# Kernel optimization log

Measured on AMD Instinct MI355X. Metric: run time of the kernel, lower is better.

The kernel has to match this reference:

```python
import jax, jax.numpy as jnp
import numpy as np

B, S, H = 64, 2048, 512


def setup_inputs() -> dict:
    key = jax.random.key(0)
    ks = jax.random.split(key, 7)
    sc = 1.0 / np.sqrt(H)
    return {
        "encoder_outputs": jax.random.normal(ks[0], (B, S, H), dtype=jnp.float32),
        "hidden": jax.random.normal(ks[1], (B, H), dtype=jnp.float32),
        "W1": jax.random.uniform(ks[2], (H, H), jnp.float32, -sc, sc),
        "b1": jax.random.uniform(ks[3], (H,), jnp.float32, -sc, sc),
        "W2": jax.random.uniform(ks[4], (H, H), jnp.float32, -sc, sc),
        "b2": jax.random.uniform(ks[5], (H,), jnp.float32, -sc, sc),
        "V": jax.random.uniform(ks[6], (H, 1), jnp.float32, -sc, sc),
        "bV": jnp.zeros((1,), dtype=jnp.float32),
    }


def reference(encoder_outputs, hidden, W1, b1, W2, b2, V, bV):
    # score: tanh(W1(enc) + W2(hidden)) ; hidden broadcast over seq dim (no repeat materialized)
    proj_enc = jnp.einsum("bsh,hk->bsk", encoder_outputs, W1) + b1          # [B,S,H]
    proj_hid = (hidden @ W2 + b2)[:, None, :]                                 # [B,1,H]
    score = jnp.tanh(proj_enc + proj_hid)                                     # [B,S,H]
    logits = jnp.einsum("bsh,hk->bsk", score, V) + bV                        # [B,S,1]
    attention_weights = jax.nn.softmax(logits, axis=1)                        # softmax over seq
    context = jnp.sum(attention_weights * encoder_outputs, axis=1)            # [B,H]
    return context, attention_weights
```

## Files before the change

### kernel.cpp

```cpp
#include <hip/hip_runtime.h>
#include <hip/hip_bf16.h>
#include <cstdint>
#include <cstddef>

#define B_ 64
#define S_ 2048
#define H_ 512

typedef __bf16 bf16x8 __attribute__((ext_vector_type(8)));
typedef float  f32x4  __attribute__((ext_vector_type(4)));

#define AS_GLB __attribute__((address_space(1)))
#define AS_LDS __attribute__((address_space(3)))

__device__ __forceinline__ float fast_tanh(float x) {
    float e = __expf(2.0f * x);
    return 1.0f - __fdividef(2.0f, e + 1.0f);
}

__global__ __launch_bounds__(256) void w1t_kernel(const float* __restrict__ W1,
                                                  unsigned short* __restrict__ Wt) {
    __shared__ float tile[32][33];
    int tn = blockIdx.x >> 4;
    int tk = blockIdx.x & 15;
    int lx = threadIdx.x & 31;
    int ly = threadIdx.x >> 5;
#pragma unroll
    for (int i = 0; i < 4; ++i) {
        int k = tk * 32 + ly + i * 8;
        tile[ly + i * 8][lx] = W1[k * H_ + tn * 32 + lx];
    }
    __syncthreads();
#pragma unroll
    for (int i = 0; i < 4; ++i) {
        int n = tn * 32 + ly + i * 8;
        float v = tile[lx][ly + i * 8];
        __bf16 bv = (__bf16)v;
        Wt[(size_t)n * H_ + tk * 32 + lx] = *(unsigned short*)&bv;
    }
}

__global__ __launch_bounds__(512) void hidproj_kernel(const float* __restrict__ hidden,
                                                      const float* __restrict__ W2,
                                                      const float* __restrict__ b1,
                                                      const float* __restrict__ b2,
                                                      float* __restrict__ cvals) {
    int b = blockIdx.x;
    int h = threadIdx.x;
    float acc = b1[h] + b2[h];
    const float* hp = hidden + b * H_;
    const float* wp = W2 + h;
#pragma unroll 8
    for (int k = 0; k < H_; ++k) acc = fmaf(hp[k], wp[(size_t)k * H_], acc);
    cvals[b * H_ + h] = acc;
}

__global__ __launch_bounds__(256) void score_kernel(const float* __restrict__ enc,
                                                    const unsigned short* __restrict__ Wt,
                                                    const float* __restrict__ cvals,
                                                    const float* __restrict__ Vp,
                                                    float* __restrict__ logits) {
    __shared__ unsigned short As[2][128][64];
    __shared__ unsigned short Bs[2][128][64];

    int orig = blockIdx.x;
    int wg   = (orig & 7) * 512 + (orig >> 3);
    int b     = wg >> 6;
    int stile = (wg >> 2) & 15;
    int ntile = wg & 3;

    int tid  = threadIdx.x;
    int wid  = tid >> 6;
    int lane = tid & 63;
    int wm = wid >> 1, wn = wid & 1;

    f32x4 acc[4][4];
#pragma unroll
    for (int m = 0; m < 4; ++m)
#pragma unroll
        for (int n = 0; n < 4; ++n) acc[m][n] = (f32x4){0.f, 0.f, 0.f, 0.f};

    const float* Abase = enc + ((size_t)(b * S_ + stile * 128)) * H_;
    float4 ra[4][2];

    auto stageA_load = [&](int kt) {
        int kk = kt * 64;
#pragma unroll
        for (int i = 0; i < 4; ++i) {
            int slot = tid + i * 256;
            int row  = slot >> 3;
            int c0   = (slot & 7) * 8;
            const float* p = Abase + (size_t)row * H_ + kk + c0;
            ra[i][0] = *(const float4*)p;
            ra[i][1] = *(const float4*)(p + 4);
        }
    };
    auto stageA_write = [&](int nb) {
#pragma unroll
        for (int i = 0; i < 4; ++i) {
            int slot = tid + i * 256;
            int row  = slot >> 3;
            int c0   = (slot & 7) * 8;
            bf16x8 v;
            const float* f = (const float*)&ra[i][0];
#pragma unroll
            for (int j = 0; j < 8; ++j) v[j] = (__bf16)f[j];
            *(bf16x8*)&As[nb][row][c0] = v;
        }
    };
    auto stageB = [&](int nb, int kt) {
        int kk = kt * 64;
#pragma unroll
        for (int i = 0; i < 4; ++i) {
            int chunk = wid * 4 + i;
            int n  = chunk * 8 + (lane >> 3);
            int c0 = (lane & 7) * 8;
            const unsigned short* src = Wt + (size_t)(ntile * 128 + n) * H_ + kk + c0;
            __builtin_amdgcn_global_load_lds((const AS_GLB unsigned int*)src,
                                             (AS_LDS unsigned int*)&Bs[nb][chunk * 8][0],
                                             16, 0, 0);
        }
    };
    auto compute = [&](int cb) {
#pragma unroll
        for (int ks = 0; ks < 2; ++ks) {
            int kof  = ks * 32 + (lane >> 4) * 8;
            int rsel = lane & 15;
            bf16x8 af[4], bfr[4];
#pragma unroll
            for (int m = 0; m < 4; ++m)
                af[m] = *(const bf16x8*)&As[cb][wm * 64 + m * 16 + rsel][kof];
#pragma unroll
            for (int n = 0; n < 4; ++n)
                bfr[n] = *(const bf16x8*)&Bs[cb][wn * 64 + n * 16 + rsel][kof];
#pragma unroll
            for (int m = 0; m < 4; ++m)
#pragma unroll
                for (int n = 0; n < 4; ++n)
                    acc[m][n] = __builtin_amdgcn_mfma_f32_16x16x32_bf16(
                        af[m], bfr[n], acc[m][n], 0, 0, 0);
        }
    };

    stageA_load(0);
    stageA_write(0);
    stageB(0, 0);
    __syncthreads();

    for (int kt = 0; kt < 8; ++kt) {
        int cur = kt & 1;
        if (kt < 7) {
            stageA_load(kt + 1);
            stageB(cur ^ 1, kt + 1);
        }
        compute(cur);
        if (kt < 7) stageA_write(cur ^ 1);
        __syncthreads();
    }

    int csel = lane & 15;
    float cw[4], vv[4];
#pragma unroll
    for (int n = 0; n < 4; ++n) {
        int col = ntile * 128 + wn * 64 + n * 16 + csel;
        cw[n] = cvals[b * H_ + col];
        vv[n] = Vp[col];
    }
    float part[16];
#pragma unroll
    for (int m = 0; m < 4; ++m)
#pragma unroll
        for (int r = 0; r < 4; ++r) {
            float p = 0.f;
#pragma unroll
            for (int n = 0; n < 4; ++n) {
                float s = fast_tanh(acc[m][n][r] + cw[n]);
                p = fmaf(vv[n], s, p);
            }
            part[m * 4 + r] = p;
        }
#pragma unroll
    for (int i = 0; i < 16; ++i)
#pragma unroll
        for (int off = 1; off < 16; off <<= 1)
            part[i] += __shfl_xor(part[i], off);

    if (csel == 0) {
        int g = lane >> 4;
#pragma unroll
        for (int m = 0; m < 4; ++m)
#pragma unroll
            for (int r = 0; r < 4; ++r) {
                int row = stile * 128 + wm * 64 + m * 16 + g * 4 + r;
                atomicAdd(&logits[b * S_ + row], part[m * 4 + r]);
            }
    }
}

__global__ __launch_bounds__(256) void softmax_kernel(const float* __restrict__ logits,
                                                      float* __restrict__ wout) {
    int b = blockIdx.x;
    int t = threadIdx.x;
    __shared__ float red[8];
    float v[8];
#pragma unroll
    for (int i = 0; i < 8; ++i) v[i] = logits[b * S_ + t + i * 256];
    float m = v[0];
#pragma unroll
    for (int i = 1; i < 8; ++i) m = fmaxf(m, v[i]);
#pragma unroll
    for (int off = 32; off >= 1; off >>= 1) m = fmaxf(m, __shfl_xor(m, off));
    int wid = t >> 6, lane = t & 63;
    if (lane == 0) red[wid] = m;
    __syncthreads();
    m = fmaxf(fmaxf(red[0], red[1]), fmaxf(red[2], red[3]));
    float s = 0.f;
#pragma unroll
    for (int i = 0; i < 8; ++i) { v[i] = __expf(v[i] - m); s += v[i]; }
#pragma unroll
    for (int off = 32; off >= 1; off >>= 1) s += __shfl_xor(s, off);
    if (lane == 0) red[4 + wid] = s;
    __syncthreads();
    float tot = red[4] + red[5] + red[6] + red[7];
    float inv = __fdividef(1.0f, tot);
#pragma unroll
    for (int i = 0; i < 8; ++i) wout[b * S_ + t + i * 256] = v[i] * inv;
}

__global__ __launch_bounds__(512) void context_kernel(const float* __restrict__ enc,
                                                      const float* __restrict__ w,
                                                      float* __restrict__ ctx) {
    int b  = blockIdx.x >> 4;
    int sc = blockIdx.x & 15;
    int h  = threadIdx.x;
    const float* ep = enc + ((size_t)(b * S_ + sc * 128)) * H_ + h;
    const float* wp = w + b * S_ + sc * 128;
    float acc = 0.f;
#pragma unroll 4
    for (int i = 0; i < 128; ++i) acc = fmaf(wp[i], ep[(size_t)i * H_], acc);
    atomicAdd(&ctx[b * H_ + h], acc);
}

extern "C" void kernel_launch(void* const* d_in, const int* in_sizes, int n_in,
                              void* d_out, int out_size, void* d_ws, size_t ws_size,
                              hipStream_t stream) {
    (void)in_sizes; (void)n_in; (void)out_size; (void)ws_size;
    const float* enc    = (const float*)d_in[0];
    const float* hidden = (const float*)d_in[1];
    const float* W1     = (const float*)d_in[2];
    const float* b1     = (const float*)d_in[3];
    const float* W2     = (const float*)d_in[4];
    const float* b2     = (const float*)d_in[5];
    const float* Vp     = (const float*)d_in[6];

    char* ws = (char*)d_ws;
    unsigned short* Wt = (unsigned short*)ws;
    float* cvals  = (float*)(ws + 524288);
    float* logits = (float*)(ws + 524288 + 131072);

    float* ctx  = (float*)d_out;
    float* wout = ctx + B_ * H_;

    hipMemsetAsync(logits, 0, (size_t)B_ * S_ * sizeof(float), stream);
    hipMemsetAsync(ctx,    0, (size_t)B_ * H_ * sizeof(float), stream);

    w1t_kernel<<<256, 256, 0, stream>>>(W1, Wt);
    hidproj_kernel<<<64, 512, 0, stream>>>(hidden, W2, b1, b2, cvals);
    score_kernel<<<4096, 256, 0, stream>>>(enc, Wt, cvals, Vp, logits);
    softmax_kernel<<<64, 256, 0, stream>>>(logits, wout);
    context_kernel<<<1024, 512, 0, stream>>>(enc, wout, ctx);
}
```

Baseline: 597.6 us.

## Load MFMA operands directly from global into registers, dropping LDS staging

The score GEMM no longer stages encoder and weight tiles through shared memory. Each lane now loads its own MFMA fragments straight from global memory into a register double buffer and converts fp32 to bf16 in registers. This removes LDS writes and reads and all block-level barriers in the k-loop. The cost is that each wave re-fetches data other waves share (A is read by both wn waves, B by both wm waves), so the kernel leans on L2/L1 caching and issues narrower, less coalesced per-row loads.

```diff
diff --git a/kernel.cpp b/kernel.cpp
--- a/kernel.cpp
+++ b/kernel.cpp
@@ -9,9 +9,6 @@
 
 typedef __bf16 bf16x8 __attribute__((ext_vector_type(8)));
 typedef float  f32x4  __attribute__((ext_vector_type(4)));
-
-#define AS_GLB __attribute__((address_space(1)))
-#define AS_LDS __attribute__((address_space(3)))
 
 __device__ __forceinline__ float fast_tanh(float x) {
     float e = __expf(2.0f * x);
@@ -60,9 +57,6 @@
                                                     const float* __restrict__ cvals,
                                                     const float* __restrict__ Vp,
                                                     float* __restrict__ logits) {
-    __shared__ unsigned short As[2][128][64];
-    __shared__ unsigned short Bs[2][128][64];
-
     int orig = blockIdx.x;
     int wg   = (orig & 7) * 512 + (orig >> 3);
     int b     = wg >> 6;
@@ -73,6 +67,8 @@
     int wid  = tid >> 6;
     int lane = tid & 63;
     int wm = wid >> 1, wn = wid & 1;
+    int rsel = lane & 15;
+    int g    = lane >> 4;
 
     f32x4 acc[4][4];
 #pragma unroll
@@ -80,82 +76,55 @@
 #pragma unroll
         for (int n = 0; n < 4; ++n) acc[m][n] = (f32x4){0.f, 0.f, 0.f, 0.f};
 
-    const float* Abase = enc + ((size_t)(b * S_ + stile * 128)) * H_;
-    float4 ra[4][2];
-
-    auto stageA_load = [&](int kt) {
-        int kk = kt * 64;
-#pragma unroll
-        for (int i = 0; i < 4; ++i) {
-            int slot = tid + i * 256;
-            int row  = slot >> 3;
-            int c0   = (slot & 7) * 8;
-            const float* p = Abase + (size_t)row * H_ + kk + c0;
-            ra[i][0] = *(const float4*)p;
-            ra[i][1] = *(const float4*)(p + 4);
+    const float* Arow[4];
+#pragma unroll
+    for (int m = 0; m < 4; ++m)
+        Arow[m] = enc + ((size_t)(b * S_ + stile * 128 + wm * 64 + m * 16 + rsel)) * H_ + g * 8;
+    const unsigned short* Brow[4];
+#pragma unroll
+    for (int n = 0; n < 4; ++n)
+        Brow[n] = Wt + ((size_t)(ntile * 128 + wn * 64 + n * 16 + rsel)) * H_ + g * 8;
+
+    float4 rA[2][4][2];
+    bf16x8 rB[2][4];
+
+#pragma unroll
+    for (int m = 0; m < 4; ++m) {
+        rA[0][m][0] = *(const float4*)(Arow[m]);
+        rA[0][m][1] = *(const float4*)(Arow[m] + 4);
+    }
+#pragma unroll
+    for (int n = 0; n < 4; ++n)
+        rB[0][n] = *(const bf16x8*)(Brow[n]);
+
+#pragma unroll
+    for (int s = 0; s < 16; ++s) {
+        const int cur = s & 1;
+        if (s < 15) {
+            const int nxt = cur ^ 1;
+            const int so  = (s + 1) * 32;
+#pragma unroll
+            for (int m = 0; m < 4; ++m) {
+                rA[nxt][m][0] = *(const float4*)(Arow[m] + so);
+                rA[nxt][m][1] = *(const float4*)(Arow[m] + so + 4);
+            }
+#pragma unroll
+            for (int n = 0; n < 4; ++n)
+                rB[nxt][n] = *(const bf16x8*)(Brow[n] + so);
         }
-    };
-    auto stageA_write = [&](int nb) {
-#pragma unroll
-        for (int i = 0; i < 4; ++i) {
-            int slot = tid + i * 256;
-            int row  = slot >> 3;
-            int c0   = (slot & 7) * 8;
-            bf16x8 v;
-            const float* f = (const float*)&ra[i][0];
-#pragma unroll
-            for (int j = 0; j < 8; ++j) v[j] = (__bf16)f[j];
-            *(bf16x8*)&As[nb][row][c0] = v;
+        bf16x8 af[4];
+#pragma unroll
+        for (int m = 0; m < 4; ++m) {
+            const float* f = (const float*)&rA[cur][m][0];
+#pragma unroll
+            for (int j = 0; j < 8; ++j) af[m][j] = (__bf16)f[j];
         }
-    };
-    auto stageB = [&](int nb, int kt) {
-        int kk = kt * 64;
-#pragma unroll
-        for (int i = 0; i < 4; ++i) {
-            int chunk = wid * 4 + i;
-            int n  = chunk * 8 + (lane >> 3);
-            int c0 = (lane & 7) * 8;
-            const unsigned short* src = Wt + (size_t)(ntile * 128 + n) * H_ + kk + c0;
-            __builtin_amdgcn_global_load_lds((const AS_GLB unsigned int*)src,
-                                             (AS_LDS unsigned int*)&Bs[nb][chunk * 8][0],
-                                             16, 0, 0);
-        }
-    };
-    auto compute = [&](int cb) {
-#pragma unroll
-        for (int ks = 0; ks < 2; ++ks) {
-            int kof  = ks * 32 + (lane >> 4) * 8;
-            int rsel = lane & 15;
-            bf16x8 af[4], bfr[4];
-#pragma unroll
-            for (int m = 0; m < 4; ++m)
-                af[m] = *(const bf16x8*)&As[cb][wm * 64 + m * 16 + rsel][kof];
+#pragma unroll
+        for (int m = 0; m < 4; ++m)
 #pragma unroll
             for (int n = 0; n < 4; ++n)
-                bfr[n] = *(const bf16x8*)&Bs[cb][wn * 64 + n * 16 + rsel][kof];
-#pragma unroll
-            for (int m = 0; m < 4; ++m)
-#pragma unroll
-                for (int n = 0; n < 4; ++n)
-                    acc[m][n] = __builtin_amdgcn_mfma_f32_16x16x32_bf16(
-                        af[m], bfr[n], acc[m][n], 0, 0, 0);
-        }
-    };
-
-    stageA_load(0);
-    stageA_write(0);
-    stageB(0, 0);
-    __syncthreads();
-
-    for (int kt = 0; kt < 8; ++kt) {
-        int cur = kt & 1;
-        if (kt < 7) {
-            stageA_load(kt + 1);
-            stageB(cur ^ 1, kt + 1);
-        }
-        compute(cur);
-        if (kt < 7) stageA_write(cur ^ 1);
-        __syncthreads();
+                acc[m][n] = __builtin_amdgcn_mfma_f32_16x16x32_bf16(
+                    af[m], rB[cur][n], acc[m][n], 0, 0, 0);
     }
 
     int csel = lane & 15;
@@ -186,12 +155,12 @@
             part[i] += __shfl_xor(part[i], off);
 
     if (csel == 0) {
-        int g = lane >> 4;
+        int gq = lane >> 4;
 #pragma unroll
         for (int m = 0; m < 4; ++m)
 #pragma unroll
             for (int r = 0; r < 4; ++r) {
-                int row = stile * 128 + wm * 64 + m * 16 + g * 4 + r;
+                int row = stile * 128 + wm * 64 + m * 16 + gq * 4 + r;
                 atomicAdd(&logits[b * S_ + row], part[m * 4 + r]);
             }
     }
```

Result: slower. 753.3 us (+26.1%).
